# Kernel optimization log

Hardware: AMD Instinct MI355X
Metric: run time of the kernel (lower is better)

The kernel has to match this reference:

```python
import jax, jax.numpy as jnp
import numpy as np

DIM = 2048
HID = 1024
E = 16
TOP_K = 2
S_SHARED = 2


def setup_inputs() -> dict:
    key = jax.random.key(0)
    ks = jax.random.split(key, 6)
    scale = 0.02
    x = jax.random.normal(ks[0], (2, 2048, DIM), dtype=jnp.float32)
    gate_w = jax.random.normal(ks[1], (DIM, E), dtype=jnp.float32) * scale
    shared_w1 = jax.random.normal(ks[2], (S_SHARED, DIM, HID), dtype=jnp.float32) * scale
    shared_w2 = jax.random.normal(ks[3], (S_SHARED, HID, DIM), dtype=jnp.float32) * scale
    w1 = jax.random.normal(ks[4], (E, DIM, HID), dtype=jnp.float32) * scale
    w2 = jax.random.normal(ks[5], (E, HID, DIM), dtype=jnp.float32) * scale
    return {"x": x, "gate_w": gate_w, "shared_w1": shared_w1,
            "shared_w2": shared_w2, "w1": w1, "w2": w2}


def reference(x, gate_w, shared_w1, shared_w2, w1, w2):
    orig_shape = x.shape
    xf = x.reshape(-1, orig_shape[-1])  # [T, D]

    # Shared experts: sum of SiLU MLPs
    hs = jax.nn.silu(jnp.einsum('td,sdh->sth', xf, shared_w1))
    shared_out = jnp.einsum('sth,shd->td', hs, shared_w2)

    # Gating
    probs = jax.nn.softmax(xf @ gate_w, axis=-1)              # [T, E]
    weights, indices = jax.lax.top_k(probs, TOP_K)            # [T, K]
    weights = weights / weights.sum(axis=-1, keepdims=True)
    aux_loss = (probs.mean(axis=0) ** 2).sum() * E

    # Combine weights per (token, expert): top_k indices are distinct
    combine = (jax.nn.one_hot(indices, E, dtype=xf.dtype) *
               weights[..., None]).sum(axis=1)                # [T, E]

    # Dense all-expert compute (reference form of gather-GEMM-scatter)
    h = jax.nn.silu(jnp.einsum('td,edh->eth', xf, w1))        # [E, T, H]
    y = jnp.einsum('eth,ehd->etd', h, w2)                     # [E, T, D]
    routed_out = jnp.einsum('te,etd->td', combine, y)         # [T, D]

    out = (shared_out + routed_out).reshape(orig_shape)
    return out, aux_loss
```

## Files before the change

kernel.cpp:

```cpp
#include <hip/hip_runtime.h>
#include <math.h>

typedef unsigned short u16;
typedef __bf16 bf16x8 __attribute__((ext_vector_type(8)));
typedef float f32x4 __attribute__((ext_vector_type(4)));

#define T_TOK 4096
#define DIMD 2048
#define HIDD 1024
#define NEXP 16
#define RMAX 12288
#define MAXBLK 96
#define BM 256
#define BN 128
#define BK 32

__device__ __forceinline__ u16 f2b(float f) {
  unsigned u = __builtin_bit_cast(unsigned, f);
  unsigned r = (u + 0x7FFFu + ((u >> 16) & 1u)) >> 16;
  return (u16)r;
}

__device__ __forceinline__ void gld16(const void* g, void* l) {
  __builtin_amdgcn_global_load_lds(
      (const __attribute__((address_space(1))) void*)g,
      (__attribute__((address_space(3))) void*)l, 16, 0, 0);
}


__global__ void k_zero(float* __restrict__ o) {
  const int i = blockIdx.x * blockDim.x + threadIdx.x;
  float4 z = {0.f, 0.f, 0.f, 0.f};
  ((float4*)o)[i] = z;
}

__global__ void k_init(int* perm, int* cnt, int* fill) {
  int i = blockIdx.x * blockDim.x + threadIdx.x;
  if (i < RMAX) perm[i] = -1;
  if (i < NEXP) { cnt[i] = 0; fill[i] = 0; }
}

__global__ void k_cvt(const float* __restrict__ x, u16* __restrict__ xb) {
  const int i = blockIdx.x * blockDim.x + threadIdx.x;
  const float4 v = ((const float4*)x)[i];
  union { u16 u[4]; unsigned long long q; } t;
  t.u[0] = f2b(v.x); t.u[1] = f2b(v.y); t.u[2] = f2b(v.z); t.u[3] = f2b(v.w);
  ((unsigned long long*)xb)[i] = t.q;
}

__global__ __launch_bounds__(256)
void k_tr(const float* __restrict__ W, u16* __restrict__ Wt,
          int K, int N, long estride, int ld_out) {
  __shared__ float t[64][65];
  const int e = blockIdx.z;
  const float* Win = W + (size_t)e * (size_t)K * (size_t)N;
  u16* Wo = Wt + (size_t)e * (size_t)estride;
  const int n0 = blockIdx.x * 64, k0 = blockIdx.y * 64;
  const int r = threadIdx.x >> 4;
  const int c = (threadIdx.x & 15) * 4;
#pragma unroll
  for (int p = 0; p < 4; ++p) {
    const int kk = p * 16 + r;
    const float4 v = *(const float4*)&Win[(size_t)(k0 + kk) * N + n0 + c];
    t[kk][c] = v.x; t[kk][c + 1] = v.y; t[kk][c + 2] = v.z; t[kk][c + 3] = v.w;
  }
  __syncthreads();
#pragma unroll
  for (int p = 0; p < 4; ++p) {
    const int nn = p * 16 + r;
    ushort4 o;
    o.x = f2b(t[c + 0][nn]); o.y = f2b(t[c + 1][nn]);
    o.z = f2b(t[c + 2][nn]); o.w = f2b(t[c + 3][nn]);
    *(ushort4*)&Wo[(size_t)(n0 + nn) * ld_out + k0 + c] = o;
  }
}

__global__ __launch_bounds__(256)
void k_gate(const float* __restrict__ x, const float* __restrict__ gw,
            int* __restrict__ top2i, float* __restrict__ top2w,
            int* __restrict__ cnt, float* __restrict__ partial) {
  const int e = threadIdx.x & 15;
  const int tt = threadIdx.x >> 4;
  const int t = blockIdx.x * 16 + tt;
  const float* xp = x + (size_t)t * DIMD;
  float acc = 0.f;
#pragma unroll 8
  for (int k = 0; k < DIMD; ++k) acc = fmaf(xp[k], gw[k * NEXP + e], acc);
  __shared__ float lg[16][17];
  __shared__ float pr[16][17];
  lg[tt][e] = acc;
  __syncthreads();
  if (e == 0) {
    float l[16];
    float mx = -1e30f;
    for (int j = 0; j < 16; ++j) { l[j] = lg[tt][j]; mx = fmaxf(mx, l[j]); }
    float s = 0.f;
    for (int j = 0; j < 16; ++j) { l[j] = expf(l[j] - mx); s += l[j]; }
    const float inv = 1.f / s;
    float p1 = -1.f, p2 = -1.f; int i1 = 0, i2 = 0;
    for (int j = 0; j < 16; ++j) {
      const float p = l[j] * inv;
      pr[tt][j] = p;
      if (p > p1) { p2 = p1; i2 = i1; p1 = p; i1 = j; }
      else if (p > p2) { p2 = p; i2 = j; }
    }
    const float wsum = p1 + p2;
    top2i[t * 2 + 0] = i1;
    top2i[t * 2 + 1] = i2;
    top2w[t * 2 + 0] = p1 / wsum;
    top2w[t * 2 + 1] = p2 / wsum;
    atomicAdd(&cnt[i1], 1);
    atomicAdd(&cnt[i2], 1);
  }
  __syncthreads();
  if (tt == 0) {
    float s = 0.f;
    for (int j = 0; j < 16; ++j) s += pr[j][e];
    partial[blockIdx.x * 16 + e] = s;
  }
}

__global__ __launch_bounds__(256)
void k_aux(const float* __restrict__ partial, float* __restrict__ auxOut) {
  __shared__ float s[16][17];
  const int e = threadIdx.x & 15, c = threadIdx.x >> 4;
  float a = 0.f;
  for (int b = c; b < 256; b += 16) a += partial[b * 16 + e];
  s[c][e] = a;
  __syncthreads();
  if (threadIdx.x == 0) {
    float aux = 0.f;
    for (int j = 0; j < 16; ++j) {
      float tot = 0.f;
      for (int cc = 0; cc < 16; ++cc) tot += s[cc][j];
      const float m = tot / (float)T_TOK;
      aux += m * m;
    }
    auxOut[0] = aux * (float)NEXP;
  }
}

__global__ void k_off(const int* __restrict__ cnt, int* __restrict__ offs,
                      int* __restrict__ tbl_e, int* __restrict__ tbl_r0,
                      int* __restrict__ nblk) {
  if (threadIdx.x != 0 || blockIdx.x != 0) return;
  int o = 0, nb = 0;
  for (int e = 0; e < NEXP; ++e) {
    offs[e] = o;
    const int b = (cnt[e] + BM - 1) / BM;
    for (int i = 0; i < b; ++i) { tbl_e[nb] = e; tbl_r0[nb] = o + i * BM; ++nb; }
    o += b * BM;
  }
  offs[NEXP] = o;
  nblk[0] = nb;
}

__global__ void k_fill(const int* __restrict__ top2i, const float* __restrict__ top2w,
                       const int* __restrict__ offs, int* __restrict__ fill,
                       int* __restrict__ perm, float* __restrict__ wrow) {
  const int id = blockIdx.x * blockDim.x + threadIdx.x;
  if (id >= T_TOK * 2) return;
  const int e = top2i[id];
  const int pos = atomicAdd(&fill[e], 1);
  const int r = offs[e] + pos;
  perm[r] = id >> 1;
  wrow[r] = top2w[id];
}

__device__ __forceinline__ void gemm_body(
    const u16* __restrict__ ap0, const u16* __restrict__ ap1,
    const u16* __restrict__ bp0, int K,
    u16* __restrict__ As, u16* __restrict__ Bs,
    int w, int lane, f32x4 (&acc)[4][4]) {
  const int aoff_st = w * 16 * BK;
  const int boff_st = w * 16 * BK;
  const int wm = w >> 1, wn = w & 1;
  const int lm = lane & 15, lq = lane >> 4;
  const int aoff_rd = (wm * 64 + lm) * BK + lq * 8;
  const int boff_rd = (wn * 64 + lm) * BK + lq * 8;
  const int nst = K / BK;

  gld16(ap0, As + aoff_st);
  gld16(ap1, As + 128 * BK + aoff_st);
  gld16(bp0, Bs + boff_st);
  __syncthreads();

  int cur = 0;
  for (int t = 1; t < nst; ++t) {
    const int k1 = t * BK;
    u16* dA = As + (cur ^ 1) * (BM * BK) + aoff_st;
    gld16(ap0 + k1, dA);
    gld16(ap1 + k1, dA + 128 * BK);
    gld16(bp0 + k1, Bs + (cur ^ 1) * (BN * BK) + boff_st);

    const u16* aR = As + cur * (BM * BK) + aoff_rd;
    const u16* bR = Bs + cur * (BN * BK) + boff_rd;
    bf16x8 af[4], bq[4];
#pragma unroll
    for (int i = 0; i < 4; ++i) af[i] = *(const bf16x8*)(aR + i * 16 * BK);
#pragma unroll
    for (int j = 0; j < 4; ++j) bq[j] = *(const bf16x8*)(bR + j * 16 * BK);
#pragma unroll
    for (int i = 0; i < 4; ++i)
#pragma unroll
      for (int j = 0; j < 4; ++j)
        acc[i][j] = __builtin_amdgcn_mfma_f32_16x16x32_bf16(af[i], bq[j], acc[i][j], 0, 0, 0);
    __syncthreads();
    cur ^= 1;
  }
  {
    const u16* aR = As + cur * (BM * BK) + aoff_rd;
    const u16* bR = Bs + cur * (BN * BK) + boff_rd;
    bf16x8 af[4], bq[4];
#pragma unroll
    for (int i = 0; i < 4; ++i) af[i] = *(const bf16x8*)(aR + i * 16 * BK);
#pragma unroll
    for (int j = 0; j < 4; ++j) bq[j] = *(const bf16x8*)(bR + j * 16 * BK);
#pragma unroll
    for (int i = 0; i < 4; ++i)
#pragma unroll
      for (int j = 0; j < 4; ++j)
        acc[i][j] = __builtin_amdgcn_mfma_f32_16x16x32_bf16(af[i], bq[j], acc[i][j], 0, 0, 0);
  }
}

__global__ __launch_bounds__(512, 4)
void k_up(const u16* __restrict__ xb, const u16* __restrict__ sw1t,
          const u16* __restrict__ w1t, u16* __restrict__ hbS,
          u16* __restrict__ hbR, const int* __restrict__ perm,
          const int* __restrict__ tbl_e, const int* __restrict__ tbl_r0,
          const int* __restrict__ nblk) {
  __shared__ u16 As[2 * BM * BK];
  __shared__ u16 Bs[2 * BN * BK];

  const int bx = blockIdx.x, by = blockIdx.y;
  const int tid = threadIdx.x;
  const int w = tid >> 6, lane = tid & 63;
  const int lr = lane >> 2;
  const int lk = (lane & 3) * 8;

  const bool routed = bx >= 32;
  int expert, r0, ga0, ga1;
  const u16* B;
  if (!routed) {
    expert = bx >> 4;
    r0 = (bx & 15) * BM;
    B = sw1t + (size_t)expert * (size_t)HIDD * DIMD;
    ga0 = r0 + w * 16 + lr;
    ga1 = r0 + 128 + w * 16 + lr;
  } else {
    const int rbx = bx - 32;
    if (rbx >= *nblk) return;
    expert = tbl_e[rbx];
    r0 = tbl_r0[rbx];
    B = w1t + (size_t)expert * (size_t)HIDD * DIMD;
    const int p0 = perm[r0 + w * 16 + lr];       ga0 = (p0 < 0) ? 0 : p0;
    const int p1 = perm[r0 + 128 + w * 16 + lr]; ga1 = (p1 < 0) ? 0 : p1;
  }

  const int n0 = by * BN;
  const u16* ap0 = xb + (size_t)ga0 * DIMD + lk;
  const u16* ap1 = xb + (size_t)ga1 * DIMD + lk;
  const u16* bp0 = B + (size_t)(n0 + w * 16 + lr) * DIMD + lk;

  f32x4 acc[4][4];
#pragma unroll
  for (int i = 0; i < 4; ++i)
#pragma unroll
    for (int j = 0; j < 4; ++j) {
      acc[i][j][0] = 0.f; acc[i][j][1] = 0.f; acc[i][j][2] = 0.f; acc[i][j][3] = 0.f;
    }

  gemm_body(ap0, ap1, bp0, DIMD, As, Bs, w, lane, acc);

  const int wm = w >> 1, wn = w & 1;
  const int lm = lane & 15, lq = lane >> 4;
#pragma unroll
  for (int i = 0; i < 4; ++i) {
#pragma unroll
    for (int r = 0; r < 4; ++r) {
      const int row = r0 + wm * 64 + i * 16 + lq * 4 + r;
      u16* dst = routed ? &hbR[(size_t)row * HIDD]
                        : &hbS[(size_t)row * DIMD + expert * HIDD];
#pragma unroll
      for (int j = 0; j < 4; ++j) {
        const int gc = n0 + wn * 64 + j * 16 + lm;
        const float v = acc[i][j][r];
        const float s = v / (1.f + expf(-v));
        dst[gc] = f2b(s);
      }
    }
  }
}

__global__ __launch_bounds__(512, 4)
void k_down(const u16* __restrict__ hbS, const u16* __restrict__ hbR,
            const u16* __restrict__ sw2ct, const u16* __restrict__ w2t,
            float* __restrict__ out, const int* __restrict__ perm,
            const float* __restrict__ wrow,
            const int* __restrict__ tbl_e, const int* __restrict__ tbl_r0,
            const int* __restrict__ nblk) {
  __shared__ u16 As[2 * BM * BK];
  __shared__ u16 Bs[2 * BN * BK];

  const int bx = blockIdx.x, by = blockIdx.y;
  const int tid = threadIdx.x;
  const int w = tid >> 6, lane = tid & 63;
  const int lr = lane >> 2;
  const int lk = (lane & 3) * 8;

  const bool routed = bx >= 16;
  int r0, K, ld;
  const u16 *Amat, *B;
  if (!routed) {
    r0 = bx * BM;
    Amat = hbS; K = DIMD; ld = DIMD;
    B = sw2ct;
  } else {
    const int rbx = bx - 16;
    if (rbx >= *nblk) return;
    const int expert = tbl_e[rbx];
    r0 = tbl_r0[rbx];
    Amat = hbR; K = HIDD; ld = HIDD;
    B = w2t + (size_t)expert * (size_t)DIMD * HIDD;
  }

  const int n0 = by * BN;
  const u16* ap0 = Amat + (size_t)(r0 + w * 16 + lr) * ld + lk;
  const u16* ap1 = Amat + (size_t)(r0 + 128 + w * 16 + lr) * ld + lk;
  const u16* bp0 = B + (size_t)(n0 + w * 16 + lr) * ld + lk;

  f32x4 acc[4][4];
#pragma unroll
  for (int i = 0; i < 4; ++i)
#pragma unroll
    for (int j = 0; j < 4; ++j) {
      acc[i][j][0] = 0.f; acc[i][j][1] = 0.f; acc[i][j][2] = 0.f; acc[i][j][3] = 0.f;
    }

  gemm_body(ap0, ap1, bp0, K, As, Bs, w, lane, acc);

  const int wm = w >> 1, wn = w & 1;
  const int lm = lane & 15, lq = lane >> 4;
#pragma unroll
  for (int i = 0; i < 4; ++i) {
#pragma unroll
    for (int r = 0; r < 4; ++r) {
      const int rr = r0 + wm * 64 + i * 16 + lq * 4 + r;
      int t; float wt;
      if (!routed) { t = rr; wt = 1.f; }
      else { t = perm[rr]; wt = (t >= 0) ? wrow[rr] : 0.f; }
      if (t >= 0) {
        float* dst = &out[(size_t)t * DIMD];
#pragma unroll
        for (int j = 0; j < 4; ++j) {
          const int gc = n0 + wn * 64 + j * 16 + lm;
          atomicAdd(&dst[gc], wt * acc[i][j][r]);
        }
      }
    }
  }
}


extern "C" void kernel_launch(void* const* d_in, const int* in_sizes, int n_in,
                              void* d_out, int out_size, void* d_ws, size_t ws_size,
                              hipStream_t stream) {
  const float* x   = (const float*)d_in[0];
  const float* gw  = (const float*)d_in[1];
  const float* sw1 = (const float*)d_in[2];
  const float* sw2 = (const float*)d_in[3];
  const float* w1  = (const float*)d_in[4];
  const float* w2  = (const float*)d_in[5];
  float* out = (float*)d_out;

  char* ws = (char*)d_ws;
  u16* xb    = (u16*)(ws);
  u16* hbS   = (u16*)(ws + (size_t)( 16 << 20));
  u16* hbR   = (u16*)(ws + (size_t)( 32 << 20));
  u16* sw1t  = (u16*)(ws + (size_t)( 56 << 20));
  u16* sw2ct = (u16*)(ws + (size_t)( 64 << 20));
  u16* w1t   = (u16*)(ws + (size_t)( 72 << 20));
  u16* w2t   = (u16*)(ws + (size_t)(136 << 20));
  char* p = ws + (size_t)(200 << 20);
  int*   top2i   = (int*)p;    p += T_TOK * 2 * 4;
  float* top2w   = (float*)p;  p += T_TOK * 2 * 4;
  int*   perm    = (int*)p;    p += RMAX * 4;
  float* wrow    = (float*)p;  p += RMAX * 4;
  int*   cnt     = (int*)p;    p += 16 * 4;
  int*   fill    = (int*)p;    p += 16 * 4;
  int*   offs    = (int*)p;    p += 32 * 4;
  int*   tbl_e   = (int*)p;    p += MAXBLK * 4;
  int*   tbl_r0  = (int*)p;    p += MAXBLK * 4;
  int*   nblk    = (int*)p;    p += 16 * 4;
  float* partial = (float*)p;  p += 256 * 16 * 4;

  k_zero<<<(T_TOK * DIMD / 4) / 256, 256, 0, stream>>>(out);
  k_init<<<(RMAX + 255) / 256, 256, 0, stream>>>(perm, cnt, fill);
  k_cvt<<<(T_TOK * DIMD / 4) / 256, 256, 0, stream>>>(x, xb);
  k_gate<<<T_TOK / 16, 256, 0, stream>>>(x, gw, top2i, top2w, cnt, partial);
  k_off<<<1, 64, 0, stream>>>(cnt, offs, tbl_e, tbl_r0, nblk);
  k_fill<<<(T_TOK * 2 + 255) / 256, 256, 0, stream>>>(top2i, top2w, offs, fill, perm, wrow);
  k_aux<<<1, 256, 0, stream>>>(partial, out + (size_t)T_TOK * DIMD);

  k_tr<<<dim3(1024 / 64, 2048 / 64,  2), 256, 0, stream>>>(sw1, sw1t, 2048, 1024, 1024l * 2048, 2048);
  k_tr<<<dim3(2048 / 64, 1024 / 64,  2), 256, 0, stream>>>(sw2, sw2ct, 1024, 2048, 1024, 2048);
  k_tr<<<dim3(1024 / 64, 2048 / 64, 16), 256, 0, stream>>>(w1, w1t, 2048, 1024, 1024l * 2048, 2048);
  k_tr<<<dim3(2048 / 64, 1024 / 64, 16), 256, 0, stream>>>(w2, w2t, 1024, 2048, 2048l * 1024, 1024);

  k_up<<<dim3(32 + 48, 8), 512, 0, stream>>>(xb, sw1t, w1t, hbS, hbR,
                                             perm, tbl_e, tbl_r0, nblk);
  k_down<<<dim3(16 + 48, 16), 512, 0, stream>>>(hbS, hbR, sw2ct, w2t, out,
                                                perm, wrow, tbl_e, tbl_r0, nblk);
}
```

Before: 834.1 us.

## Retile MoE GEMMs to 128x256x64 with swizzled LDS and deeper pipeline

Changes the grouped GEMM tiles from 256x128x32 to 128x256x64 and stores LDS tiles with an XOR swizzle to avoid bank conflicts. It replaces the double-buffer loop with a two-stage prefetch pipeline that uses explicit vmcnt waits, raw barriers and s_setprio around the MFMA bursts. Routed blocks are now 128 rows, which cuts padding waste, and the grid grows to MAXBLK blocks. The cost is more LDS per block (96KB), fewer resident blocks per CU, and a dependence on hand-tuned waitcnt ordering being correct.

```diff
diff --git a/kernel.cpp b/kernel.cpp
--- a/kernel.cpp
+++ b/kernel.cpp
@@ -9,11 +9,11 @@
 #define DIMD 2048
 #define HIDD 1024
 #define NEXP 16
-#define RMAX 12288
+#define RMAX 10240
 #define MAXBLK 96
-#define BM 256
-#define BN 128
-#define BK 32
+#define BM 128
+#define BN 256
+#define BK 64
 
 __device__ __forceinline__ u16 f2b(float f) {
   unsigned u = __builtin_bit_cast(unsigned, f);
@@ -167,102 +167,125 @@
   wrow[r] = top2w[id];
 }
 
-__device__ __forceinline__ void gemm_body(
-    const u16* __restrict__ ap0, const u16* __restrict__ ap1,
-    const u16* __restrict__ bp0, int K,
-    u16* __restrict__ As, u16* __restrict__ Bs,
-    int w, int lane, f32x4 (&acc)[4][4]) {
-  const int aoff_st = w * 16 * BK;
-  const int boff_st = w * 16 * BK;
-  const int wm = w >> 1, wn = w & 1;
-  const int lm = lane & 15, lq = lane >> 4;
-  const int aoff_rd = (wm * 64 + lm) * BK + lq * 8;
-  const int boff_rd = (wn * 64 + lm) * BK + lq * 8;
-  const int nst = K / BK;
-
-  gld16(ap0, As + aoff_st);
-  gld16(ap1, As + 128 * BK + aoff_st);
-  gld16(bp0, Bs + boff_st);
-  __syncthreads();
-
-  int cur = 0;
-  for (int t = 1; t < nst; ++t) {
-    const int k1 = t * BK;
-    u16* dA = As + (cur ^ 1) * (BM * BK) + aoff_st;
-    gld16(ap0 + k1, dA);
-    gld16(ap1 + k1, dA + 128 * BK);
-    gld16(bp0 + k1, Bs + (cur ^ 1) * (BN * BK) + boff_st);
-
-    const u16* aR = As + cur * (BM * BK) + aoff_rd;
-    const u16* bR = Bs + cur * (BN * BK) + boff_rd;
-    bf16x8 af[4], bq[4];
-#pragma unroll
-    for (int i = 0; i < 4; ++i) af[i] = *(const bf16x8*)(aR + i * 16 * BK);
-#pragma unroll
-    for (int j = 0; j < 4; ++j) bq[j] = *(const bf16x8*)(bR + j * 16 * BK);
+
+__device__ __forceinline__ void stage_tile(
+    const u16* gA0, const u16* gA1, const u16* gB0, const u16* gB1,
+    const u16* gB2, const u16* gB3, int k0, u16* S, int b, int w) {
+  u16* As = S + b * 24576;
+  u16* Bs = As + 8192;
+  gld16(gA0 + k0, As + w * 512);
+  gld16(gA1 + k0, As + 4096 + w * 512);
+  gld16(gB0 + k0, Bs + w * 512);
+  gld16(gB1 + k0, Bs + 4096 + w * 512);
+  gld16(gB2 + k0, Bs + 8192 + w * 512);
+  gld16(gB3 + k0, Bs + 12288 + w * 512);
+}
+
+__device__ __forceinline__ void comp_tile(const u16* __restrict__ S, int b,
+    const int (&aoff)[4][2], const int (&boff)[4][2], f32x4 (&acc)[4][4]) {
+  const u16* As = S + b * 24576;
+  const u16* Bs = As + 8192;
+#pragma unroll
+  for (int kh = 0; kh < 2; ++kh) {
+    bf16x8 a[4], bq[4];
+#pragma unroll
+    for (int i = 0; i < 4; ++i) a[i] = *(const bf16x8*)(As + aoff[i][kh]);
+#pragma unroll
+    for (int j = 0; j < 4; ++j) bq[j] = *(const bf16x8*)(Bs + boff[j][kh]);
+    __builtin_amdgcn_s_setprio(1);
 #pragma unroll
     for (int i = 0; i < 4; ++i)
 #pragma unroll
       for (int j = 0; j < 4; ++j)
-        acc[i][j] = __builtin_amdgcn_mfma_f32_16x16x32_bf16(af[i], bq[j], acc[i][j], 0, 0, 0);
-    __syncthreads();
-    cur ^= 1;
-  }
-  {
-    const u16* aR = As + cur * (BM * BK) + aoff_rd;
-    const u16* bR = Bs + cur * (BN * BK) + boff_rd;
-    bf16x8 af[4], bq[4];
-#pragma unroll
-    for (int i = 0; i < 4; ++i) af[i] = *(const bf16x8*)(aR + i * 16 * BK);
-#pragma unroll
-    for (int j = 0; j < 4; ++j) bq[j] = *(const bf16x8*)(bR + j * 16 * BK);
-#pragma unroll
-    for (int i = 0; i < 4; ++i)
-#pragma unroll
-      for (int j = 0; j < 4; ++j)
-        acc[i][j] = __builtin_amdgcn_mfma_f32_16x16x32_bf16(af[i], bq[j], acc[i][j], 0, 0, 0);
-  }
-}
-
-__global__ __launch_bounds__(512, 4)
+        acc[i][j] = __builtin_amdgcn_mfma_f32_16x16x32_bf16(a[i], bq[j], acc[i][j], 0, 0, 0);
+    __builtin_amdgcn_s_setprio(0);
+  }
+}
+
+#define FENCE asm volatile("" ::: "memory")
+#define VMW6  asm volatile("s_waitcnt vmcnt(6)" ::: "memory")
+#define VMW0  asm volatile("s_waitcnt vmcnt(0)" ::: "memory")
+
+__device__ __forceinline__ void gemm_pipe(
+    const u16* gA0, const u16* gA1, const u16* gB0, const u16* gB1,
+    const u16* gB2, const u16* gB3, int K, u16* S,
+    const int (&aoff)[4][2], const int (&boff)[4][2],
+    f32x4 (&acc)[4][4], int w) {
+  const int nt = K >> 6;
+  stage_tile(gA0, gA1, gB0, gB1, gB2, gB3, 0, S, 0, w);
+  stage_tile(gA0, gA1, gB0, gB1, gB2, gB3, 64, S, 1, w);
+  VMW6;
+  __builtin_amdgcn_s_barrier();
+  FENCE;
+  for (int t = 0; t < nt - 2; ++t) {
+    comp_tile(S, t & 1, aoff, boff, acc);
+    FENCE;
+    __builtin_amdgcn_s_barrier();
+    FENCE;
+    stage_tile(gA0, gA1, gB0, gB1, gB2, gB3, (t + 2) << 6, S, t & 1, w);
+    VMW6;
+    __builtin_amdgcn_s_barrier();
+    FENCE;
+  }
+  comp_tile(S, 0, aoff, boff, acc);
+  VMW0;
+  __builtin_amdgcn_s_barrier();
+  FENCE;
+  comp_tile(S, 1, aoff, boff, acc);
+}
+
+__global__ __launch_bounds__(512, 2)
 void k_up(const u16* __restrict__ xb, const u16* __restrict__ sw1t,
           const u16* __restrict__ w1t, u16* __restrict__ hbS,
           u16* __restrict__ hbR, const int* __restrict__ perm,
           const int* __restrict__ tbl_e, const int* __restrict__ tbl_r0,
           const int* __restrict__ nblk) {
-  __shared__ u16 As[2 * BM * BK];
-  __shared__ u16 Bs[2 * BN * BK];
-
+  __shared__ u16 S[49152];
   const int bx = blockIdx.x, by = blockIdx.y;
   const int tid = threadIdx.x;
   const int w = tid >> 6, lane = tid & 63;
-  const int lr = lane >> 2;
-  const int lk = (lane & 3) * 8;
+  const int lm = lane & 15, lq = lane >> 4;
+  const int wm = w >> 2, wn = w & 3;
+  const int srow = w * 8 + (lane >> 3);
+  const int c8 = lane & 7;
 
   const bool routed = bx >= 32;
-  int expert, r0, ga0, ga1;
-  const u16* B;
+  int r0, ga0, ga1;
+  const u16* Bb;
   if (!routed) {
-    expert = bx >> 4;
-    r0 = (bx & 15) * BM;
-    B = sw1t + (size_t)expert * (size_t)HIDD * DIMD;
-    ga0 = r0 + w * 16 + lr;
-    ga1 = r0 + 128 + w * 16 + lr;
+    r0 = bx * BM;
+    Bb = sw1t;
+    ga0 = r0 + srow; ga1 = r0 + 64 + srow;
   } else {
+    if (by >= 4) return;
     const int rbx = bx - 32;
     if (rbx >= *nblk) return;
-    expert = tbl_e[rbx];
+    const int e = tbl_e[rbx];
     r0 = tbl_r0[rbx];
-    B = w1t + (size_t)expert * (size_t)HIDD * DIMD;
-    const int p0 = perm[r0 + w * 16 + lr];       ga0 = (p0 < 0) ? 0 : p0;
-    const int p1 = perm[r0 + 128 + w * 16 + lr]; ga1 = (p1 < 0) ? 0 : p1;
-  }
-
+    Bb = w1t + (size_t)e * (size_t)HIDD * DIMD;
+    const int p0 = perm[r0 + srow];      ga0 = (p0 < 0) ? 0 : p0;
+    const int p1 = perm[r0 + 64 + srow]; ga1 = (p1 < 0) ? 0 : p1;
+  }
   const int n0 = by * BN;
-  const u16* ap0 = xb + (size_t)ga0 * DIMD + lk;
-  const u16* ap1 = xb + (size_t)ga1 * DIMD + lk;
-  const u16* bp0 = B + (size_t)(n0 + w * 16 + lr) * DIMD + lk;
-
+  const u16* gA0 = xb + (size_t)ga0 * DIMD + (c8 ^ ((srow >> 1) & 7)) * 8;
+  const u16* gA1 = xb + (size_t)ga1 * DIMD + (c8 ^ (((64 + srow) >> 1) & 7)) * 8;
+  const u16* gB[4];
+#pragma unroll
+  for (int p = 0; p < 4; ++p) {
+    const int n = p * 64 + srow;
+    gB[p] = Bb + (size_t)(n0 + n) * DIMD + (c8 ^ ((n >> 1) & 7)) * 8;
+  }
+  int aoff[4][2], boff[4][2];
+#pragma unroll
+  for (int i = 0; i < 4; ++i) {
+    const int m = wm * 64 + i * 16 + lm;
+    const int n = wn * 64 + i * 16 + lm;
+#pragma unroll
+    for (int kh = 0; kh < 2; ++kh) {
+      aoff[i][kh] = m * 64 + (((kh << 2) | lq) ^ ((m >> 1) & 7)) * 8;
+      boff[i][kh] = n * 64 + (((kh << 2) | lq) ^ ((n >> 1) & 7)) * 8;
+    }
+  }
   f32x4 acc[4][4];
 #pragma unroll
   for (int i = 0; i < 4; ++i)
@@ -271,17 +294,14 @@
       acc[i][j][0] = 0.f; acc[i][j][1] = 0.f; acc[i][j][2] = 0.f; acc[i][j][3] = 0.f;
     }
 
-  gemm_body(ap0, ap1, bp0, DIMD, As, Bs, w, lane, acc);
-
-  const int wm = w >> 1, wn = w & 1;
-  const int lm = lane & 15, lq = lane >> 4;
+  gemm_pipe(gA0, gA1, gB[0], gB[1], gB[2], gB[3], DIMD, S, aoff, boff, acc, w);
+
 #pragma unroll
   for (int i = 0; i < 4; ++i) {
 #pragma unroll
     for (int r = 0; r < 4; ++r) {
       const int row = r0 + wm * 64 + i * 16 + lq * 4 + r;
-      u16* dst = routed ? &hbR[(size_t)row * HIDD]
-                        : &hbS[(size_t)row * DIMD + expert * HIDD];
+      u16* dst = routed ? &hbR[(size_t)row * HIDD] : &hbS[(size_t)row * DIMD];
 #pragma unroll
       for (int j = 0; j < 4; ++j) {
         const int gc = n0 + wn * 64 + j * 16 + lm;
@@ -293,43 +313,57 @@
   }
 }
 
-__global__ __launch_bounds__(512, 4)
+__global__ __launch_bounds__(512, 2)
 void k_down(const u16* __restrict__ hbS, const u16* __restrict__ hbR,
             const u16* __restrict__ sw2ct, const u16* __restrict__ w2t,
             float* __restrict__ out, const int* __restrict__ perm,
             const float* __restrict__ wrow,
             const int* __restrict__ tbl_e, const int* __restrict__ tbl_r0,
             const int* __restrict__ nblk) {
-  __shared__ u16 As[2 * BM * BK];
-  __shared__ u16 Bs[2 * BN * BK];
-
+  __shared__ u16 S[49152];
   const int bx = blockIdx.x, by = blockIdx.y;
   const int tid = threadIdx.x;
   const int w = tid >> 6, lane = tid & 63;
-  const int lr = lane >> 2;
-  const int lk = (lane & 3) * 8;
-
-  const bool routed = bx >= 16;
+  const int lm = lane & 15, lq = lane >> 4;
+  const int wm = w >> 2, wn = w & 3;
+  const int srow = w * 8 + (lane >> 3);
+  const int c8 = lane & 7;
+
+  const bool routed = bx >= 32;
   int r0, K, ld;
-  const u16 *Amat, *B;
+  const u16 *Ab, *Bb;
   if (!routed) {
     r0 = bx * BM;
-    Amat = hbS; K = DIMD; ld = DIMD;
-    B = sw2ct;
+    Ab = hbS; K = DIMD; ld = DIMD;
+    Bb = sw2ct;
   } else {
-    const int rbx = bx - 16;
+    const int rbx = bx - 32;
     if (rbx >= *nblk) return;
-    const int expert = tbl_e[rbx];
+    const int e = tbl_e[rbx];
     r0 = tbl_r0[rbx];
-    Amat = hbR; K = HIDD; ld = HIDD;
-    B = w2t + (size_t)expert * (size_t)DIMD * HIDD;
-  }
-
+    Ab = hbR; K = HIDD; ld = HIDD;
+    Bb = w2t + (size_t)e * (size_t)DIMD * HIDD;
+  }
   const int n0 = by * BN;
-  const u16* ap0 = Amat + (size_t)(r0 + w * 16 + lr) * ld + lk;
-  const u16* ap1 = Amat + (size_t)(r0 + 128 + w * 16 + lr) * ld + lk;
-  const u16* bp0 = B + (size_t)(n0 + w * 16 + lr) * ld + lk;
-
+  const u16* gA0 = Ab + (size_t)(r0 + srow) * ld + (c8 ^ ((srow >> 1) & 7)) * 8;
+  const u16* gA1 = Ab + (size_t)(r0 + 64 + srow) * ld + (c8 ^ (((64 + srow) >> 1) & 7)) * 8;
+  const u16* gB[4];
+#pragma unroll
+  for (int p = 0; p < 4; ++p) {
+    const int n = p * 64 + srow;
+    gB[p] = Bb + (size_t)(n0 + n) * ld + (c8 ^ ((n >> 1) & 7)) * 8;
+  }
+  int aoff[4][2], boff[4][2];
+#pragma unroll
+  for (int i = 0; i < 4; ++i) {
+    const int m = wm * 64 + i * 16 + lm;
+    const int n = wn * 64 + i * 16 + lm;
+#pragma unroll
+    for (int kh = 0; kh < 2; ++kh) {
+      aoff[i][kh] = m * 64 + (((kh << 2) | lq) ^ ((m >> 1) & 7)) * 8;
+      boff[i][kh] = n * 64 + (((kh << 2) | lq) ^ ((n >> 1) & 7)) * 8;
+    }
+  }
   f32x4 acc[4][4];
 #pragma unroll
   for (int i = 0; i < 4; ++i)
@@ -338,10 +372,8 @@
       acc[i][j][0] = 0.f; acc[i][j][1] = 0.f; acc[i][j][2] = 0.f; acc[i][j][3] = 0.f;
     }
 
-  gemm_body(ap0, ap1, bp0, K, As, Bs, w, lane, acc);
-
-  const int wm = w >> 1, wn = w & 1;
-  const int lm = lane & 15, lq = lane >> 4;
+  gemm_pipe(gA0, gA1, gB[0], gB[1], gB[2], gB[3], K, S, aoff, boff, acc, w);
+
 #pragma unroll
   for (int i = 0; i < 4; ++i) {
 #pragma unroll
@@ -408,8 +440,8 @@
   k_tr<<<dim3(1024 / 64, 2048 / 64, 16), 256, 0, stream>>>(w1, w1t, 2048, 1024, 1024l * 2048, 2048);
   k_tr<<<dim3(2048 / 64, 1024 / 64, 16), 256, 0, stream>>>(w2, w2t, 1024, 2048, 2048l * 1024, 1024);
 
-  k_up<<<dim3(32 + 48, 8), 512, 0, stream>>>(xb, sw1t, w1t, hbS, hbR,
-                                             perm, tbl_e, tbl_r0, nblk);
-  k_down<<<dim3(16 + 48, 16), 512, 0, stream>>>(hbS, hbR, sw2ct, w2t, out,
-                                                perm, wrow, tbl_e, tbl_r0, nblk);
-}
+  k_up<<<dim3(32 + MAXBLK, 8), 512, 0, stream>>>(xb, sw1t, w1t, hbS, hbR,
+                                                 perm, tbl_e, tbl_r0, nblk);
+  k_down<<<dim3(32 + MAXBLK, 8), 512, 0, stream>>>(hbS, hbR, sw2ct, w2t, out,
+                                                   perm, wrow, tbl_e, tbl_r0, nblk);
+}
```

Measured after the change: 813.4 us. 1.03x faster.
